# Performance work log

Hardware: AMD Instinct MI355X
Metric: run time of the kernel (lower is better)

## Reference

```python
import jax, jax.numpy as jnp
import numpy as np

B, T, D, N = 16, 1024, 1024, 8


def setup_inputs() -> dict:
    key = jax.random.key(0)
    k1, k2, k3, k4 = jax.random.split(key, 4)
    s = 1.0 / np.sqrt(D)
    return {
        "x": jax.random.normal(k1, (B, T, D), dtype=jnp.float32),
        "W_h": jax.random.normal(k2, (D, D), dtype=jnp.float32) * (0.9 * s),
        "W_x": jax.random.normal(k3, (D, D), dtype=jnp.float32) * s,
        "b_h": jnp.zeros((D,), dtype=jnp.float32),
        "W_write": jax.random.normal(k4, (D, D), dtype=jnp.float32) * s,
    }


def reference(x, W_h, W_x, b_h, W_write):
    Bs, Ts, Ds = x.shape
    scale = 1.0 / Ds ** 0.5
    x_proj = jnp.einsum('btd,ed->bte', x, W_x)  # x @ W_x.T
    h_tape0 = jnp.zeros((Bs, N, Ds), dtype=x.dtype)
    h_work0 = jnp.zeros((Bs, Ds), dtype=x.dtype)

    def step(carry, x_t):
        h_tape, h_work = carry
        read_scores = jnp.einsum('bd,bnd->bn', h_work, h_tape) * scale
        read_attn = jax.nn.softmax(read_scores, axis=-1)
        read_val = jnp.einsum('bn,bnd->bd', read_attn, h_tape)
        Rh = h_work @ W_h.T
        h_work_new = jnp.tanh(x_t + Rh + read_val + b_h)
        write_val = h_work_new @ W_write.T
        write_scores = jnp.einsum('bd,bnd->bn', write_val, h_tape) * scale
        write_attn = jax.nn.softmax(write_scores, axis=-1)
        wa = write_attn[..., None]  # [B,N,1]
        h_tape_new = h_tape * (1.0 - wa) + write_val[:, None, :] * wa
        return (h_tape_new, h_work_new), h_work_new

    (h_tape_final, _), h_work_all = jax.lax.scan(
        step, (h_tape0, h_work0), jnp.swapaxes(x_proj, 0, 1))
    h_work_all = jnp.swapaxes(h_work_all, 0, 1)  # [B,T,D]
    return h_work_all, h_tape_final, h_work_all[:, -1, :]
```

## Files before the change

### kernel.cpp

```cpp
#include <hip/hip_runtime.h>
#include <math.h>

typedef __bf16 bf16x8 __attribute__((ext_vector_type(8)));
typedef float f32x4 __attribute__((ext_vector_type(4)));

namespace {

constexpr int kB = 16;
constexpr int kT = 1024;
constexpr int kD = 1024;
constexpr int kN = 8;
constexpr float kScale = 0.03125f;

constexpr unsigned long long kSent = ~0ull;
constexpr unsigned kSentW = 0xFFFFFFFFu;
constexpr int kHS = 3 * kB * kD;
constexpr int kRW = 2 * kB * kD;

__device__ inline unsigned short f2bf(float f) {
  unsigned u = __float_as_uint(f);
  u += 0x7FFFu + ((u >> 16) & 1u);
  return (unsigned short)(u >> 16);
}
__device__ inline float bf2f(unsigned short b) {
  return __uint_as_float(((unsigned)b) << 16);
}

__device__ inline void atst8(void* p, unsigned long long v) {
  __hip_atomic_store((unsigned long long*)p, v, __ATOMIC_RELAXED,
                     __HIP_MEMORY_SCOPE_AGENT);
}
__device__ inline unsigned long long atld8(const void* p) {
  return __hip_atomic_load((unsigned long long*)p, __ATOMIC_RELAXED,
                           __HIP_MEMORY_SCOPE_AGENT);
}
__device__ inline void atstf(float* p, float v) {
  __hip_atomic_store(p, v, __ATOMIC_RELAXED, __HIP_MEMORY_SCOPE_AGENT);
}
__device__ inline void atstu(unsigned* p, unsigned v) {
  __hip_atomic_store(p, v, __ATOMIC_RELAXED, __HIP_MEMORY_SCOPE_AGENT);
}
__device__ inline unsigned atldu(const unsigned* p) {
  return __hip_atomic_load((unsigned*)p, __ATOMIC_RELAXED,
                           __HIP_MEMORY_SCOPE_AGENT);
}

union U16 { unsigned long long ll[2]; unsigned wrd[4]; bf16x8 bv; float4 f4; };

__global__ __launch_bounds__(256)
void xproj_kernel(const float* __restrict__ X, const float* __restrict__ Wx,
                  float* __restrict__ C) {
  __shared__ float Xs[16][132];
  __shared__ float Ws[16][132];
  const int tid = threadIdx.x;
  const int n0 = blockIdx.x * 128;
  const int m0 = blockIdx.y * 128;
  const int tx = tid & 15;
  const int ty = tid >> 4;
  const int lr = tid >> 2;
  const int lc = (tid & 3) * 4;

  float acc[8][8];
#pragma unroll
  for (int i = 0; i < 8; ++i)
#pragma unroll
    for (int j = 0; j < 8; ++j) acc[i][j] = 0.f;

  for (int k0 = 0; k0 < kD; k0 += 16) {
    const float4 xa = *(const float4*)&X[(size_t)(m0 + lr) * kD + k0 + lc];
    const float4 xb = *(const float4*)&X[(size_t)(m0 + lr + 64) * kD + k0 + lc];
    const float4 wa = *(const float4*)&Wx[(size_t)(n0 + lr) * kD + k0 + lc];
    const float4 wb = *(const float4*)&Wx[(size_t)(n0 + lr + 64) * kD + k0 + lc];
    __syncthreads();
    Xs[lc + 0][lr] = xa.x; Xs[lc + 1][lr] = xa.y; Xs[lc + 2][lr] = xa.z; Xs[lc + 3][lr] = xa.w;
    Xs[lc + 0][lr + 64] = xb.x; Xs[lc + 1][lr + 64] = xb.y; Xs[lc + 2][lr + 64] = xb.z; Xs[lc + 3][lr + 64] = xb.w;
    Ws[lc + 0][lr] = wa.x; Ws[lc + 1][lr] = wa.y; Ws[lc + 2][lr] = wa.z; Ws[lc + 3][lr] = wa.w;
    Ws[lc + 0][lr + 64] = wb.x; Ws[lc + 1][lr + 64] = wb.y; Ws[lc + 2][lr + 64] = wb.z; Ws[lc + 3][lr + 64] = wb.w;
    __syncthreads();
#pragma unroll
    for (int k = 0; k < 16; ++k) {
      float a[8], b[8];
      *(float4*)&a[0] = *(const float4*)&Xs[k][ty * 8];
      *(float4*)&a[4] = *(const float4*)&Xs[k][ty * 8 + 4];
      *(float4*)&b[0] = *(const float4*)&Ws[k][tx * 8];
      *(float4*)&b[4] = *(const float4*)&Ws[k][tx * 8 + 4];
#pragma unroll
      for (int i = 0; i < 8; ++i)
#pragma unroll
        for (int j = 0; j < 8; ++j) acc[i][j] += a[i] * b[j];
    }
  }
#pragma unroll
  for (int i = 0; i < 8; ++i) {
    float4 v0 = make_float4(acc[i][0], acc[i][1], acc[i][2], acc[i][3]);
    float4 v1 = make_float4(acc[i][4], acc[i][5], acc[i][6], acc[i][7]);
    float* p = &C[(size_t)(m0 + ty * 8 + i) * kD + n0 + tx * 8];
    *(float4*)p = v0;
    *(float4*)(p + 4) = v1;
  }
}

__device__ inline void store_split(unsigned short* hs, int b, int d4, float4 h) {
  union { unsigned short u[4]; unsigned long long ll; } c2, c1, c0;
  float hv[4] = {h.x, h.y, h.z, h.w};
#pragma unroll
  for (int e = 0; e < 4; ++e) {
    unsigned short x = f2bf(hv[e]);
    float r = hv[e] - bf2f(x);
    unsigned short y = f2bf(r);
    float r2 = r - bf2f(y);
    unsigned short z = f2bf(r2);
    c2.u[e] = x; c1.u[e] = y; c0.u[e] = z;
  }
  const int w = d4 >> 8;
  const int j = (d4 >> 5) & 7;
  const int q = (d4 >> 3) & 3;
  const int hf = (d4 >> 2) & 1;
  const int off = ((w * 8 + j) << 9) + (hf << 8) + ((q * 16 + b) << 2);
  atst8(&hs[0 * 16384 + off], c2.ll);
  atst8(&hs[1 * 16384 + off], c1.ll);
  atst8(&hs[2 * 16384 + off], c0.ll);
}

__global__ __launch_bounds__(256, 1)
void scan_kernel(const float* __restrict__ Wh, const float* __restrict__ Ww,
                 const float* __restrict__ bh,
                 float* __restrict__ hall,
                 unsigned short* __restrict__ hsplit,
                 float* __restrict__ rw,
                 unsigned* __restrict__ hmark,
                 float* __restrict__ out_tape,
                 float* __restrict__ out_h) {
  const int g = blockIdx.x;
  const int tid = threadIdx.x;
  const int w = tid >> 6;
  const int ln = tid & 63;
  const int bat = ln & 15;
  const int q = ln >> 4;
  const bool tapeb = (g < kB);
  const int col0 = (g & 31) * 32;
  const int matw = g >> 5;

  __shared__ float tp[kN][kD];
  __shared__ f32x4 Cred[2][4][2][64];
  __shared__ float red2[4][16];

  bf16x8 wf[3][2][8];
  {
    const float* Wsrc = matw ? Ww : Wh;
#pragma unroll
    for (int ct = 0; ct < 2; ++ct)
#pragma unroll
      for (int j = 0; j < 8; ++j) {
        const float* src = &Wsrc[(size_t)(col0 + ct * 16 + bat) * kD + (w * 8 + j) * 32 + q * 8];
        float v[8];
        *(float4*)&v[0] = *(const float4*)src;
        *(float4*)&v[4] = *(const float4*)(src + 4);
        union { unsigned short u[8]; bf16x8 b; } e2, e1, e0;
#pragma unroll
        for (int e = 0; e < 8; ++e) {
          unsigned short a = f2bf(v[e]);
          float r = v[e] - bf2f(a);
          unsigned short b2 = f2bf(r);
          float r2 = r - bf2f(b2);
          unsigned short c = f2bf(r2);
          e2.u[e] = a; e1.u[e] = b2; e0.u[e] = c;
        }
        wf[0][ct][j] = e2.b;
        wf[1][ct][j] = e1.b;
        wf[2][ct][j] = e0.b;
      }
  }

  float4 hprev = make_float4(0.f, 0.f, 0.f, 0.f);
  float4 bh4 = make_float4(0.f, 0.f, 0.f, 0.f);
  const int d4 = tid * 4;
  if (tapeb) {
    const size_t x0 = (size_t)g * kT * kD + d4;
    float4 xp0 = *(const float4*)&hall[x0];
    hprev.x = tanhf(xp0.x); hprev.y = tanhf(xp0.y);
    hprev.z = tanhf(xp0.z); hprev.w = tanhf(xp0.w);
    *(float4*)&hall[x0] = hprev;
    store_split(hsplit, g, d4, hprev);
    asm volatile("s_waitcnt vmcnt(0)" ::: "memory");
    if (ln == 0) atstu(&hmark[(w * 16 + g) * 16], 1u);
    bh4 = *(const float4*)&bh[d4];
    float4 z = make_float4(0.f, 0.f, 0.f, 0.f);
#pragma unroll
    for (int i = 0; i < 8; ++i) ((float4*)&tp[0][0])[i * 256 + tid] = z;
    __syncthreads();
  }

  for (int t = 0; t < kT; ++t) {
    const int p = t & 1;
    const unsigned short* hb = hsplit + p * kHS;

    float4 xp4 = make_float4(0.f, 0.f, 0.f, 0.f);
    if (tapeb && t < kT - 1)
      xp4 = *(const float4*)&hall[((size_t)g * kT + (t + 1)) * kD + d4];

    {
      const unsigned need = (unsigned)(t + 1);
      const unsigned* mk = &hmark[(w * 16 + bat) * 16];
      for (;;) {
        unsigned v = 0;
        if (q == 0) v = atldu(mk);
        v = __shfl(v, bat);
        if (v >= need) break;
        __builtin_amdgcn_s_sleep(1);
      }
      asm volatile("" ::: "memory");
    }
    U16 uf[3][8];
    const unsigned short* hw0 = hb + (w << 12) + (ln << 2);
    for (;;) {
      int bad = 0;
#pragma unroll
      for (int j = 0; j < 8; ++j) {
        const unsigned short* p0 = hw0 + (j << 9);
#pragma unroll
        for (int part = 0; part < 3; ++part) {
          uf[part][j].ll[0] = atld8(p0 + part * 16384);
          uf[part][j].ll[1] = atld8(p0 + part * 16384 + 256);
        }
      }
#pragma unroll
      for (int j = 0; j < 8; ++j)
#pragma unroll
        for (int part = 0; part < 3; ++part)
          bad |= (uf[part][j].ll[0] == kSent) | (uf[part][j].ll[1] == kSent);
      if (!bad) break;
      __builtin_amdgcn_s_sleep(1);
    }
    asm volatile("" ::: "memory");

    f32x4 zf = {0.f, 0.f, 0.f, 0.f};
    f32x4 acc[2][2] = {{zf, zf}, {zf, zf}};
#pragma unroll
    for (int j = 0; j < 8; ++j) {
      const int s = j & 1;
#pragma unroll
      for (int ct = 0; ct < 2; ++ct) {
        f32x4 a = acc[ct][s];
        a = __builtin_amdgcn_mfma_f32_16x16x32_bf16(uf[0][j].bv, wf[0][ct][j], a, 0, 0, 0);
        a = __builtin_amdgcn_mfma_f32_16x16x32_bf16(uf[0][j].bv, wf[1][ct][j], a, 0, 0, 0);
        a = __builtin_amdgcn_mfma_f32_16x16x32_bf16(uf[1][j].bv, wf[0][ct][j], a, 0, 0, 0);
        a = __builtin_amdgcn_mfma_f32_16x16x32_bf16(uf[0][j].bv, wf[2][ct][j], a, 0, 0, 0);
        a = __builtin_amdgcn_mfma_f32_16x16x32_bf16(uf[2][j].bv, wf[0][ct][j], a, 0, 0, 0);
        a = __builtin_amdgcn_mfma_f32_16x16x32_bf16(uf[1][j].bv, wf[1][ct][j], a, 0, 0, 0);
        acc[ct][s] = a;
      }
    }
    Cred[p][w][0][ln] = acc[0][0] + acc[0][1];
    Cred[p][w][1][ln] = acc[1][0] + acc[1][1];
    __syncthreads();
    if (tid < 128) {
      const int ct = tid >> 6, l2 = tid & 63;
      f32x4 sv = Cred[p][0][ct][l2] + Cred[p][1][ct][l2] +
                 Cred[p][2][ct][l2] + Cred[p][3][ct][l2];
      float* dst = rw + p * kRW + matw * (kB * kD);
      const int col = col0 + ct * 16 + (l2 & 15);
      const int m0 = (l2 >> 4) * 4;
#pragma unroll
      for (int r = 0; r < 4; ++r) atstf(&dst[(size_t)(m0 + r) * kD + col], sv[r]);
    }

    if (!tapeb) continue;

    const int b = g;
    float* rwp = rw + p * kRW;
    float* pr = &rwp[b * kD + d4];
    float* pw = &rwp[kB * kD + b * kD + d4];
    float4 rh4, wv4;
    for (;;) {
      U16 ur, uw;
      ur.ll[0] = atld8(pr); ur.ll[1] = atld8(pr + 2);
      uw.ll[0] = atld8(pw); uw.ll[1] = atld8(pw + 2);
      int bad = 0;
#pragma unroll
      for (int k2 = 0; k2 < 4; ++k2)
        bad |= (ur.wrd[k2] == kSentW) | (uw.wrd[k2] == kSentW);
      if (!bad) { rh4 = ur.f4; wv4 = uw.f4; break; }
      __builtin_amdgcn_s_sleep(1);
    }
    asm volatile("" ::: "memory");
    atst8(pr, kSent); atst8(pr + 2, kSent);
    atst8(pw, kSent); atst8(pw + 2, kSent);

    float part[kN];
#pragma unroll
    for (int n = 0; n < kN; ++n) {
      const float4 tv = *(const float4*)&tp[n][d4];
      part[n] = wv4.x * tv.x + wv4.y * tv.y + wv4.z * tv.z + wv4.w * tv.w;
    }
#pragma unroll
    for (int off = 32; off > 0; off >>= 1)
#pragma unroll
      for (int n = 0; n < kN; ++n) part[n] += __shfl_xor(part[n], off);
    if (ln == 0)
#pragma unroll
      for (int n = 0; n < kN; ++n) red2[w][n] = part[n];
    __syncthreads();

    {
      unsigned short* hp0 = hsplit + p * kHS;
      const int off = (((d4 >> 8) * 8 + ((d4 >> 5) & 7)) << 9) +
                      (((d4 >> 2) & 1) << 8) + ((((d4 >> 3) & 3) * 16 + b) << 2);
      atst8(&hp0[0 * 16384 + off], kSent);
      atst8(&hp0[1 * 16384 + off], kSent);
      atst8(&hp0[2 * 16384 + off], kSent);
    }

    float wa[kN];
    {
      float mx = -1e30f;
#pragma unroll
      for (int n = 0; n < kN; ++n) {
        const float sc = kScale * (red2[0][n] + red2[1][n] + red2[2][n] + red2[3][n]);
        wa[n] = sc;
        mx = fmaxf(mx, sc);
      }
      float ssum = 0.f;
#pragma unroll
      for (int n = 0; n < kN; ++n) { wa[n] = expf(wa[n] - mx); ssum += wa[n]; }
      const float inv = 1.f / ssum;
#pragma unroll
      for (int n = 0; n < kN; ++n) wa[n] *= inv;
    }

#pragma unroll
    for (int n = 0; n < kN; ++n) {
      float4 tv = *(const float4*)&tp[n][d4];
      const float wn = wa[n], om = 1.f - wn;
      tv.x = tv.x * om + wv4.x * wn; tv.y = tv.y * om + wv4.y * wn;
      tv.z = tv.z * om + wv4.z * wn; tv.w = tv.w * om + wv4.w * wn;
      *(float4*)&tp[n][d4] = tv;
    }

    if (t == kT - 1) {
#pragma unroll
      for (int n = 0; n < kN; ++n) {
        const float4 tv = *(const float4*)&tp[n][d4];
        *(float4*)&out_tape[((size_t)b * kN + n) * kD + d4] = tv;
      }
      *(float4*)&out_h[b * kD + d4] = hprev;
      continue;
    }

#pragma unroll
    for (int n = 0; n < kN; ++n) {
      const float4 tv = *(const float4*)&tp[n][d4];
      part[n] = hprev.x * tv.x + hprev.y * tv.y + hprev.z * tv.z + hprev.w * tv.w;
    }
#pragma unroll
    for (int off = 32; off > 0; off >>= 1)
#pragma unroll
      for (int n = 0; n < kN; ++n) part[n] += __shfl_xor(part[n], off);
    if (ln == 0)
#pragma unroll
      for (int n = 0; n < kN; ++n) red2[w][8 + n] = part[n];
    __syncthreads();

    float ra[kN];
    {
      float mx = -1e30f;
#pragma unroll
      for (int n = 0; n < kN; ++n) {
        const float sc = kScale * (red2[0][8 + n] + red2[1][8 + n] + red2[2][8 + n] + red2[3][8 + n]);
        ra[n] = sc;
        mx = fmaxf(mx, sc);
      }
      float ssum = 0.f;
#pragma unroll
      for (int n = 0; n < kN; ++n) { ra[n] = expf(ra[n] - mx); ssum += ra[n]; }
      const float inv = 1.f / ssum;
#pragma unroll
      for (int n = 0; n < kN; ++n) ra[n] *= inv;
    }

    float4 rv = make_float4(0.f, 0.f, 0.f, 0.f);
#pragma unroll
    for (int n = 0; n < kN; ++n) {
      const float4 tv = *(const float4*)&tp[n][d4];
      rv.x += ra[n] * tv.x; rv.y += ra[n] * tv.y;
      rv.z += ra[n] * tv.z; rv.w += ra[n] * tv.w;
    }

    float4 hn;
    hn.x = tanhf(xp4.x + rh4.x + rv.x + bh4.x);
    hn.y = tanhf(xp4.y + rh4.y + rv.y + bh4.y);
    hn.z = tanhf(xp4.z + rh4.z + rv.z + bh4.z);
    hn.w = tanhf(xp4.w + rh4.w + rv.w + bh4.w);

    asm volatile("s_waitcnt vmcnt(0)" ::: "memory");
    store_split(hsplit + (p ^ 1) * kHS, b, d4, hn);
    if (ln == 0) atstu(&hmark[(w * 16 + b) * 16], (unsigned)(t + 2));
    *(float4*)&hall[((size_t)b * kT + (t + 1)) * kD + d4] = hn;
    hprev = hn;
  }
}

}

extern "C" void kernel_launch(void* const* d_in, const int* in_sizes, int n_in,
                              void* d_out, int out_size, void* d_ws, size_t ws_size,
                              hipStream_t stream) {
  const float* x  = (const float*)d_in[0];
  const float* Wh = (const float*)d_in[1];
  const float* Wx = (const float*)d_in[2];
  const float* bh = (const float*)d_in[3];
  const float* Ww = (const float*)d_in[4];

  float* out = (float*)d_out;
  float* hall = out;
  float* out_tape = out + (size_t)kB * kT * kD;
  float* out_h = out_tape + (size_t)kB * kN * kD;

  unsigned* hmark = (unsigned*)d_ws;
  unsigned short* hsplit = (unsigned short*)((char*)d_ws + 4096);
  float* rw = (float*)((char*)d_ws + 4096 + 2 * kHS * (int)sizeof(unsigned short));

  hipMemsetAsync(d_ws, 0, 4096, stream);
  hipMemsetAsync((char*)d_ws + 4096, 0xFF,
                 2 * kHS * sizeof(unsigned short) + 2 * kRW * sizeof(float),
                 stream);

  xproj_kernel<<<dim3(kD / 128, (kB * kT) / 128), 256, 0, stream>>>(x, Wx, hall);

  scan_kernel<<<64, 256, 0, stream>>>(Wh, Ww, bh, hall, hsplit, rw, hmark,
                                      out_tape, out_h);
}
```

Before: 10.08 ms.

## Derive read scores algebraically from pre-update tape dots, removing a barrier

Computes the h_prev·tape dot products before waiting on the matvec results, and adds an h_prev·write_val dot to the write-score reduction. The read scores after the tape update are then rebuilt in closed form as (1-wa)*s_h + wa*s_hwv, which removes the second reduction pass and its __syncthreads from the serial critical path. The hmark progress signal is also moved earlier, and the vmcnt(0) wait before the split store is dropped. This changes floating-point rounding order and may weaken the memory-ordering guarantees between the split store and the marker signal.

```diff
diff --git a/kernel.cpp b/kernel.cpp
--- a/kernel.cpp
+++ b/kernel.cpp
@@ -143,7 +143,7 @@
 
   __shared__ float tp[kN][kD];
   __shared__ f32x4 Cred[2][4][2][64];
-  __shared__ float red2[4][16];
+  __shared__ float red2[4][20];
 
   bf16x8 wf[3][2][8];
   {
@@ -271,6 +271,23 @@
     float* rwp = rw + p * kRW;
     float* pr = &rwp[b * kD + d4];
     float* pw = &rwp[kB * kD + b * kD + d4];
+
+    {
+      float ph[kN];
+#pragma unroll
+      for (int n = 0; n < kN; ++n) {
+        const float4 tv = *(const float4*)&tp[n][d4];
+        ph[n] = hprev.x * tv.x + hprev.y * tv.y + hprev.z * tv.z + hprev.w * tv.w;
+      }
+#pragma unroll
+      for (int off = 32; off > 0; off >>= 1)
+#pragma unroll
+        for (int n = 0; n < kN; ++n) ph[n] += __shfl_xor(ph[n], off);
+      if (ln == 0)
+#pragma unroll
+        for (int n = 0; n < kN; ++n) red2[w][8 + n] = ph[n];
+    }
+
     float4 rh4, wv4;
     for (;;) {
       U16 ur, uw;
@@ -287,19 +304,24 @@
     atst8(pr, kSent); atst8(pr + 2, kSent);
     atst8(pw, kSent); atst8(pw + 2, kSent);
 
-    float part[kN];
-#pragma unroll
-    for (int n = 0; n < kN; ++n) {
-      const float4 tv = *(const float4*)&tp[n][d4];
-      part[n] = wv4.x * tv.x + wv4.y * tv.y + wv4.z * tv.z + wv4.w * tv.w;
-    }
-#pragma unroll
-    for (int off = 32; off > 0; off >>= 1)
-#pragma unroll
-      for (int n = 0; n < kN; ++n) part[n] += __shfl_xor(part[n], off);
-    if (ln == 0)
-#pragma unroll
-      for (int n = 0; n < kN; ++n) red2[w][n] = part[n];
+    {
+      float pv[9];
+#pragma unroll
+      for (int n = 0; n < kN; ++n) {
+        const float4 tv = *(const float4*)&tp[n][d4];
+        pv[n] = wv4.x * tv.x + wv4.y * tv.y + wv4.z * tv.z + wv4.w * tv.w;
+      }
+      pv[8] = hprev.x * wv4.x + hprev.y * wv4.y + hprev.z * wv4.z + hprev.w * wv4.w;
+#pragma unroll
+      for (int off = 32; off > 0; off >>= 1)
+#pragma unroll
+        for (int n = 0; n < 9; ++n) pv[n] += __shfl_xor(pv[n], off);
+      if (ln == 0) {
+#pragma unroll
+        for (int n = 0; n < kN; ++n) red2[w][n] = pv[n];
+        red2[w][16] = pv[8];
+      }
+    }
     __syncthreads();
 
     {
@@ -311,6 +333,7 @@
       atst8(&hp0[2 * 16384 + off], kSent);
     }
 
+    float s_h[kN], s_hwv;
     float wa[kN];
     {
       float mx = -1e30f;
@@ -319,7 +342,9 @@
         const float sc = kScale * (red2[0][n] + red2[1][n] + red2[2][n] + red2[3][n]);
         wa[n] = sc;
         mx = fmaxf(mx, sc);
-      }
+        s_h[n] = red2[0][8 + n] + red2[1][8 + n] + red2[2][8 + n] + red2[3][8 + n];
+      }
+      s_hwv = red2[0][16] + red2[1][16] + red2[2][16] + red2[3][16];
       float ssum = 0.f;
 #pragma unroll
       for (int n = 0; n < kN; ++n) { wa[n] = expf(wa[n] - mx); ssum += wa[n]; }
@@ -337,6 +362,8 @@
       *(float4*)&tp[n][d4] = tv;
     }
 
+    if (ln == 0) atstu(&hmark[(w * 16 + b) * 16], (unsigned)(t + 2));
+
     if (t == kT - 1) {
 #pragma unroll
       for (int n = 0; n < kN; ++n) {
@@ -347,26 +374,12 @@
       continue;
     }
 
-#pragma unroll
-    for (int n = 0; n < kN; ++n) {
-      const float4 tv = *(const float4*)&tp[n][d4];
-      part[n] = hprev.x * tv.x + hprev.y * tv.y + hprev.z * tv.z + hprev.w * tv.w;
-    }
-#pragma unroll
-    for (int off = 32; off > 0; off >>= 1)
-#pragma unroll
-      for (int n = 0; n < kN; ++n) part[n] += __shfl_xor(part[n], off);
-    if (ln == 0)
-#pragma unroll
-      for (int n = 0; n < kN; ++n) red2[w][8 + n] = part[n];
-    __syncthreads();
-
     float ra[kN];
     {
       float mx = -1e30f;
 #pragma unroll
       for (int n = 0; n < kN; ++n) {
-        const float sc = kScale * (red2[0][8 + n] + red2[1][8 + n] + red2[2][8 + n] + red2[3][8 + n]);
+        const float sc = kScale * (s_h[n] * (1.f - wa[n]) + s_hwv * wa[n]);
         ra[n] = sc;
         mx = fmaxf(mx, sc);
       }
@@ -392,9 +405,7 @@
     hn.z = tanhf(xp4.z + rh4.z + rv.z + bh4.z);
     hn.w = tanhf(xp4.w + rh4.w + rv.w + bh4.w);
 
-    asm volatile("s_waitcnt vmcnt(0)" ::: "memory");
     store_split(hsplit + (p ^ 1) * kHS, b, d4, hn);
-    if (ln == 0) atstu(&hmark[(w * 16 + b) * 16], (unsigned)(t + 2));
     *(float4*)&hall[((size_t)b * kT + (t + 1)) * kD + d4] = hn;
     hprev = hn;
   }
```

Result: slower. 10.99 ms (+9.0%).
